# Kernel optimization log

Hardware: AMD Instinct MI355X
Metric: run time of the kernel (lower is better)

## Reference

```python
import jax, jax.numpy as jnp
import numpy as np

B, L, D = 2, 2048, 1024
H, QK, V = 8, 128, 128
EPS = 1e-5  # torch GroupNorm default


def setup_inputs() -> dict:
    key = jax.random.key(0)
    ks = jax.random.split(key, 6)
    sequence = jax.random.normal(ks[0], (B, L, D), jnp.float32)
    times = jnp.broadcast_to(jnp.arange(L, dtype=jnp.float32), (B, L))
    shift = D ** -0.5
    scale = 2.0 * shift
    w_q = jax.random.uniform(ks[1], (H, D, QK), jnp.float32) * scale - shift
    w_k = jax.random.uniform(ks[2], (H, D, QK), jnp.float32) * scale - shift
    w_v = jax.random.uniform(ks[3], (H, D, V), jnp.float32) * scale - shift
    out_dims = H * V
    w_g = jax.random.uniform(ks[4], (D, out_dims), jnp.float32) * scale - shift
    shift2 = out_dims ** -0.5
    scale2 = 2.0 * shift2
    w_o = jax.random.uniform(ks[5], (out_dims, out_dims), jnp.float32) * scale2 - shift2
    gn_w = jnp.ones((out_dims,), jnp.float32)
    gn_b = jnp.zeros((out_dims,), jnp.float32)
    return dict(sequence=sequence, times=times, w_q=w_q, w_k=w_k, w_v=w_v,
                w_g=w_g, w_o=w_o, gn_w=gn_w, gn_b=gn_b)


def rotate_by_i(x):
    # pairs (even, odd) -> (-odd, even), interleaved back
    x2 = x.reshape(x.shape[:-1] + (-1, 2))
    real, imag = x2[..., 0], x2[..., 1]
    return jnp.stack([-imag, real], axis=-1).reshape(x.shape)


def reference(sequence, times, w_q, w_k, w_v, w_g, w_o, gn_w, gn_b):
    gammas = 1.0 - 2.0 ** (-5.0 - jnp.arange(H, dtype=jnp.float32))            # (H,)
    thetas = 10000.0 ** (-2.0 * jnp.arange(QK // 2, dtype=jnp.float32) / QK)   # (QK/2,)

    q = jnp.einsum('bld,hdk->hblk', sequence, w_q)  # (H,B,L,QK)
    k = jnp.einsum('bld,hdk->hblk', sequence, w_k)
    v = jnp.einsum('bld,hdv->hblv', sequence, w_v)  # (H,B,L,V)

    # xPos rotor: angles interleaved-duplicated along last dim
    angles = times[..., None] * thetas              # (B,L,QK/2)
    cos = jnp.repeat(jnp.cos(angles), 2, axis=-1)   # (B,L,QK)
    sin = jnp.repeat(jnp.sin(angles), 2, axis=-1)
    q = cos * q + sin * rotate_by_i(q)
    k = cos * k - sin * rotate_by_i(k)

    # causal exponential-decay mask D[n,m] = gamma**(n-m) * (n>=m)
    mat = times[:, :, None] - times[:, None, :]     # (B,L,L)
    mask = mat >= 0
    g4 = gammas[:, None, None, None]                # (H,1,1,1)
    d = jnp.where(mask, g4 ** jnp.where(mask, mat, 0.0), 0.0)  # (H,B,L,L)

    ret = jnp.einsum('hbik,hbjk->hbij', q, k) * d   # (H,B,L,L)
    retention = jnp.einsum('hbij,hbjv->hbiv', ret, v)  # (H,B,L,V)

    # GroupNorm(num_heads, H*V): normalize each head's V channels per token
    r = jnp.transpose(retention, (1, 2, 0, 3))      # (B,L,H,V)
    mean = r.mean(-1, keepdims=True)
    var = r.var(-1, keepdims=True)
    rn = (r - mean) / jnp.sqrt(var + EPS)
    rn = rn * gn_w.reshape(H, V) + gn_b.reshape(H, V)
    rn = rn.reshape(B, L, H * V)

    g = sequence @ w_g
    gate = g * jax.nn.sigmoid(g)                    # swish
    return (gate * rn) @ w_o                        # (B,L,H*V)
```

## Files before the change

kernel.cpp:

```cpp
#include <hip/hip_runtime.h>
#include <stdint.h>

typedef unsigned short u16;
typedef unsigned int   u32;
typedef short  short8 __attribute__((ext_vector_type(8)));
typedef float  f32x4  __attribute__((ext_vector_type(4)));

#define DEV static __device__ __forceinline__

DEV float bf2f(u16 u) { u32 x = ((u32)u) << 16; float f; __builtin_memcpy(&f, &x, 4); return f; }
DEV u16 f2bf(float f) {
  u32 u; __builtin_memcpy(&u, &f, 4);
  return (u16)((u + 0x7FFFu + ((u >> 16) & 1u)) >> 16);
}
DEV bool probe_bf16(const void* times) { return *(const u32*)times == 0x3F800000u; }

DEV void gload16(const u16* g, u16* l) {
  __builtin_amdgcn_global_load_lds(
      (__attribute__((address_space(1))) void*)(u16*)g,
      (__attribute__((address_space(3))) void*)l, 16, 0, 0);
}

DEV f32x4 MFMA(short8 a, short8 b, f32x4 c) {
  return __builtin_amdgcn_mfma_f32_16x16x32_bf16(a, b, c, 0, 0, 0);
}

DEV void gemm128(const u16* Ag, const u16* Bg, int K, u16* sA, u16* sB,
                 f32x4 (&acc)[4][4]) {
  const int tid = threadIdx.x;
  const int lane = tid & 63, w = tid >> 6;
  const int wm = w >> 1, wn = w & 1;
  const int row = lane & 15, quad = lane >> 4;
  f32x4 z = {0.f, 0.f, 0.f, 0.f};
#pragma unroll
  for (int mt = 0; mt < 4; ++mt)
#pragma unroll
    for (int nt = 0; nt < 4; ++nt) acc[mt][nt] = z;

  for (int k0 = 0; k0 < K; k0 += 64) {
    __syncthreads();
#pragma unroll
    for (int i = 0; i < 4; ++i) {
      int c = (w << 2) + i;
      gload16(Ag + (size_t)(c * 8 + (lane >> 3)) * K + k0 + (lane & 7) * 8, sA + c * 544);
      gload16(Bg + (size_t)(c * 8 + (lane >> 3)) * K + k0 + (lane & 7) * 8, sB + c * 544);
    }
    __syncthreads();
#pragma unroll
    for (int kt = 0; kt < 2; ++kt) {
      short8 av[4], bv[4];
#pragma unroll
      for (int t = 0; t < 4; ++t) {
        int m = wm * 64 + t * 16 + row;
        av[t] = *(const short8*)(sA + (m >> 3) * 544 + (m & 7) * 64 + kt * 32 + quad * 8);
        int n = wn * 64 + t * 16 + row;
        bv[t] = *(const short8*)(sB + (n >> 3) * 544 + (n & 7) * 64 + kt * 32 + quad * 8);
      }
#pragma unroll
      for (int mt = 0; mt < 4; ++mt)
#pragma unroll
        for (int nt = 0; nt < 4; ++nt)
          acc[mt][nt] = MFMA(av[mt], bv[nt], acc[mt][nt]);
    }
  }
}

__global__ __launch_bounds__(256) void transpose_kernel(
    const void* wq, const void* wk, const void* wv, const void* wg,
    const void* wo, const void* times, u16* wsT) {
  __shared__ u16 T[128 * 132];
  int s = blockIdx.x, t = blockIdx.y;
  bool isbf = probe_bf16(times);
  const void* src; int ld; size_t off0;
  if (s < 8)       { src = wq; ld = 128;  off0 = (size_t)s * 131072; }
  else if (s < 16) { src = wk; ld = 128;  off0 = (size_t)(s - 8) * 131072; }
  else if (s < 24) { src = wv; ld = 128;  off0 = (size_t)(s - 16) * 131072; }
  else if (s < 32) { src = wg; ld = 1024; off0 = (size_t)(s - 24) * 128; }
  else             { src = wo; ld = 1024; off0 = (size_t)(s - 32) * 128; }
  int d0 = t * 128;
  const u16* s16 = (const u16*)src;
  const float* s32 = (const float*)src;
  for (int pass = 0; pass < 64; ++pass) {
    int idx = pass * 256 + threadIdx.x;
    int dl = idx >> 7, c = idx & 127;
    size_t goff = off0 + (size_t)(d0 + dl) * ld + c;
    T[c * 132 + dl] = isbf ? s16[goff] : f2bf(s32[goff]);
  }
  __syncthreads();
  u16* dst = wsT + (size_t)s * 131072;
  for (int pass = 0; pass < 16; ++pass) {
    int idx = pass * 256 + threadIdx.x;
    int c = idx >> 5, ch = idx & 31;
    uint2 v = *(const uint2*)&T[c * 132 + ch * 4];
    *(uint2*)&dst[(size_t)c * 1024 + d0 + ch * 4] = v;
  }
}

__global__ __launch_bounds__(256) void seq_kernel(const void* seq, const void* times, u16* dst) {
  bool isbf = probe_bf16(times);
  size_t idx = ((size_t)blockIdx.x * 256 + threadIdx.x) * 8;
  if (isbf) {
    *(uint4*)&dst[idx] = *(const uint4*)((const u16*)seq + idx);
  } else {
    const float* s = (const float*)seq;
    u32 a0 = (u32)f2bf(s[idx + 0]) | ((u32)f2bf(s[idx + 1]) << 16);
    u32 a1 = (u32)f2bf(s[idx + 2]) | ((u32)f2bf(s[idx + 3]) << 16);
    u32 a2 = (u32)f2bf(s[idx + 4]) | ((u32)f2bf(s[idx + 5]) << 16);
    u32 a3 = (u32)f2bf(s[idx + 6]) | ((u32)f2bf(s[idx + 7]) << 16);
    uint4 v; v.x = a0; v.y = a1; v.z = a2; v.w = a3;
    *(uint4*)&dst[idx] = v;
  }
}

__global__ __launch_bounds__(256, 4) void proj_kernel(
    const u16* seqb, const void* times, const u16* wsT,
    u16* qws, u16* kws, u16* vtws, u16* gatews) {
  __shared__ __align__(16) u16 smem[17408];
  u16* sA = smem;
  u16* sB = smem + 8704;
  int nb = blockIdx.x, mb = blockIdx.y;
  f32x4 acc[4][4];
  gemm128(seqb + (size_t)mb * 128 * 1024, wsT + (size_t)nb * 131072, 1024, sA, sB, acc);

  const int tid = threadIdx.x, lane = tid & 63, w = tid >> 6;
  const int wm = w >> 1, wn = w & 1, row = lane & 15, quad = lane >> 4;
  const bool isbf = probe_bf16(times);
  const u16* t16 = (const u16*)times;
  const float* t32 = (const float*)times;
  const int b = mb >> 4, l0 = (mb & 15) * 128;

  __syncthreads();

  if (nb < 16) {
    int type = nb >> 3;
    int h = nb & 7;
    float sgnk = type ? -1.f : 1.f;
#pragma unroll
    for (int mt = 0; mt < 4; ++mt) {
#pragma unroll
      for (int nt = 0; nt < 4; ++nt) {
        int c = wn * 64 + nt * 16 + row;
        float theta = exp2f(-0.2076205059304601f * (float)(c >> 1));
        float sgn = (c & 1) ? 1.f : -1.f;
#pragma unroll
        for (int r = 0; r < 4; ++r) {
          int lloc = wm * 64 + mt * 16 + quad * 4 + r;
          float v = acc[mt][nt][r];
          float pv = __shfl_xor(v, 1);
          float tv = isbf ? bf2f(t16[b * 2048 + l0 + lloc]) : t32[b * 2048 + l0 + lloc];
          float rev = theta * tv * 0.15915494309189535f;
          rev -= floorf(rev);
          float sn = __builtin_amdgcn_sinf(rev);
          float cs = __builtin_amdgcn_cosf(rev);
          float ov = cs * v + sgnk * sgn * sn * pv;
          u16 o16 = f2bf(ov);
          int other = __shfl_xor((int)o16, 1);
          if (!(lane & 1))
            *(u32*)&smem[lloc * 136 + c] = (u32)o16 | ((u32)other << 16);
        }
      }
    }
    __syncthreads();
    u16* outp = (type ? kws : qws) + (((size_t)(h * 2 + b) * 2048 + l0) << 7);
#pragma unroll
    for (int p = 0; p < 8; ++p) {
      int idx = p * 256 + tid, rr = idx >> 4, ch = idx & 15;
      *(uint4*)&outp[(size_t)rr * 128 + ch * 8] = *(const uint4*)&smem[rr * 136 + ch * 8];
    }
  } else if (nb < 24) {
    int h = nb & 7;
#pragma unroll
    for (int mt = 0; mt < 4; ++mt) {
      int lb = wm * 64 + mt * 16 + quad * 4;
#pragma unroll
      for (int nt = 0; nt < 4; ++nt) {
        int c = wn * 64 + nt * 16 + row;
        uint2 pk;
        pk.x = (u32)f2bf(acc[mt][nt][0]) | ((u32)f2bf(acc[mt][nt][1]) << 16);
        pk.y = (u32)f2bf(acc[mt][nt][2]) | ((u32)f2bf(acc[mt][nt][3]) << 16);
        *(uint2*)&smem[c * 136 + lb] = pk;
      }
    }
    __syncthreads();
    u16* outp = vtws + (size_t)(h * 2 + b) * 262144 + l0;
#pragma unroll
    for (int p = 0; p < 8; ++p) {
      int idx = p * 256 + tid, cc = idx >> 4, ch = idx & 15;
      *(uint4*)&outp[(size_t)cc * 2048 + ch * 8] = *(const uint4*)&smem[cc * 136 + ch * 8];
    }
  } else {
    int cb = nb - 24;
#pragma unroll
    for (int mt = 0; mt < 4; ++mt) {
#pragma unroll
      for (int nt = 0; nt < 4; ++nt) {
        int c = wn * 64 + nt * 16 + row;
#pragma unroll
        for (int r = 0; r < 4; ++r) {
          int lloc = wm * 64 + mt * 16 + quad * 4 + r;
          float x = acc[mt][nt][r];
          float s = x / (1.f + __expf(-x));
          u16 o16 = f2bf(s);
          int other = __shfl_xor((int)o16, 1);
          if (!(lane & 1))
            *(u32*)&smem[lloc * 136 + c] = (u32)o16 | ((u32)other << 16);
        }
      }
    }
    __syncthreads();
    u16* outp = gatews + (size_t)(mb * 128) * 1024 + (size_t)cb * 128;
#pragma unroll
    for (int p = 0; p < 8; ++p) {
      int idx = p * 256 + tid, rr = idx >> 4, ch = idx & 15;
      *(uint4*)&outp[(size_t)rr * 1024 + ch * 8] = *(const uint4*)&smem[rr * 136 + ch * 8];
    }
  }
}

__global__ __launch_bounds__(256) void retention_kernel(
    const u16* qws, const u16* kws, const u16* vtws, const void* times,
    float* rws, float* part0, float* part1) {
  __shared__ __align__(16) u16 sP[4][1280];
  const int tid = threadIdx.x, lane = tid & 63, w = tid >> 6;
  const int row = lane & 15, quad = lane >> 4;
  u16* myP = &sP[w][0];

  const int bx = blockIdx.x;
  const int xcd = bx & 7, slot = bx >> 3;
  const int hb = xcd + ((slot >> 5) << 3);
  const int cid = 125 - ((slot & 31) * 4 + w);
  if (cid < 0) return;
  int itile, idx, nc;
  if (cid < 22)      { itile = cid; idx = 0; nc = 1; }
  else if (cid < 66) { itile = 22 + ((cid - 22) >> 1); idx = (cid - 22) & 1; nc = 2; }
  else { int x = cid - 66; int q3 = (x * 171) >> 9; itile = 44 + q3; idx = x - 3 * q3; nc = 3; }
  const int n = itile + 1;
  int lo, hi;
  if (nc == 1)      { lo = 0;                      hi = n; }
  else if (nc == 2) { lo = (idx * n) >> 1;         hi = ((idx + 1) * n) >> 1; }
  else              { lo = (idx * n * 171) >> 9;   hi = ((idx + 1) * n * 171) >> 9; }

  const int h = hb >> 1, b = hb & 1;
  const int i0 = itile * 32;
  const bool isbf = probe_bf16(times);
  const u16* t16 = (const u16*)times + b * 2048;
  const float* t32 = (const float*)times + b * 2048;
  const float gamma = 1.f - exp2f(-5.f - (float)h);
  const float l2g = log2f(gamma);

  short8 qf[2][4];
  const u16* qbase = qws + ((size_t)hb * 2048 + i0) * 128;
#pragma unroll
  for (int ii = 0; ii < 2; ++ii)
#pragma unroll
    for (int kt = 0; kt < 4; ++kt)
      qf[ii][kt] = *(const short8*)(qbase + (size_t)(ii * 16 + row) * 128 + kt * 32 + quad * 8);

  float tiv[2];
#pragma unroll
  for (int ii = 0; ii < 2; ++ii)
    tiv[ii] = isbf ? bf2f(t16[i0 + ii * 16 + row]) : t32[i0 + ii * 16 + row];

  f32x4 z = {0.f, 0.f, 0.f, 0.f};
  f32x4 oacc[2][8];
#pragma unroll
  for (int mt = 0; mt < 2; ++mt)
#pragma unroll
    for (int vt = 0; vt < 8; ++vt) oacc[mt][vt] = z;

  const u16* kbase = kws + (size_t)hb * 262144;
  const u16* vbase = vtws + (size_t)hb * 262144;

  for (int jt = lo; jt < hi; ++jt) {
    const int j0 = jt * 32;
    if (l2g * (float)(i0 - j0 - 47) < -57.f) continue;

    f32x4 pt[2][2];
#pragma unroll
    for (int jj = 0; jj < 2; ++jj)
#pragma unroll
      for (int ii = 0; ii < 2; ++ii) pt[jj][ii] = z;
#pragma unroll
    for (int kt = 0; kt < 4; ++kt) {
      short8 kf0 = *(const short8*)(kbase + (size_t)(j0 + row) * 128 + kt * 32 + quad * 8);
      short8 kf1 = *(const short8*)(kbase + (size_t)(j0 + 16 + row) * 128 + kt * 32 + quad * 8);
      pt[0][0] = MFMA(kf0, qf[0][kt], pt[0][0]);
      pt[0][1] = MFMA(kf0, qf[1][kt], pt[0][1]);
      pt[1][0] = MFMA(kf1, qf[0][kt], pt[1][0]);
      pt[1][1] = MFMA(kf1, qf[1][kt], pt[1][1]);
    }

    const float j0f = (float)j0;
    const float rpo0 = exp2f(l2g * (tiv[0] - j0f));
    const float rpo1 = exp2f(l2g * (tiv[1] - j0f));
    const bool diag = (jt == itile);
#pragma unroll
    for (int jj = 0; jj < 2; ++jj) {
      float tj[4];
      if (isbf) {
        uint2 tp = *(const uint2*)&t16[j0 + jj * 16 + quad * 4];
        tj[0] = bf2f((u16)tp.x); tj[1] = bf2f((u16)(tp.x >> 16));
        tj[2] = bf2f((u16)tp.y); tj[3] = bf2f((u16)(tp.y >> 16));
      } else {
        f32x4 tp = *(const f32x4*)&t32[j0 + jj * 16 + quad * 4];
        tj[0] = tp[0]; tj[1] = tp[1]; tj[2] = tp[2]; tj[3] = tp[3];
      }
      float cp[4];
#pragma unroll
      for (int r = 0; r < 4; ++r) cp[r] = exp2f(l2g * (j0f - tj[r]));
#pragma unroll
      for (int ii = 0; ii < 2; ++ii) {
        float rp = ii ? rpo1 : rpo0;
        float ti = tiv[ii];
        float v0 = pt[jj][ii][0] * rp * cp[0];
        float v1 = pt[jj][ii][1] * rp * cp[1];
        float v2 = pt[jj][ii][2] * rp * cp[2];
        float v3 = pt[jj][ii][3] * rp * cp[3];
        if (diag) {
          if (ti < tj[0]) v0 = 0.f;
          if (ti < tj[1]) v1 = 0.f;
          if (ti < tj[2]) v2 = 0.f;
          if (ti < tj[3]) v3 = 0.f;
        }
        uint2 pk;
        pk.x = (u32)f2bf(v0) | ((u32)f2bf(v1) << 16);
        pk.y = (u32)f2bf(v2) | ((u32)f2bf(v3) << 16);
        *(uint2*)&myP[(ii * 16 + row) * 40 + jj * 16 + quad * 4] = pk;
      }
    }

    short8 a0 = *(const short8*)&myP[(row) * 40 + quad * 8];
    short8 a1 = *(const short8*)&myP[(16 + row) * 40 + quad * 8];
#pragma unroll
    for (int vt = 0; vt < 8; ++vt) {
      short8 vb = *(const short8*)(vbase + (size_t)(vt * 16 + row) * 2048 + j0 + quad * 8);
      oacc[0][vt] = MFMA(a0, vb, oacc[0][vt]);
      oacc[1][vt] = MFMA(a1, vb, oacc[1][vt]);
    }
  }

  float* dst;
  if (idx == 0) {
    dst = rws + ((size_t)hb * 2048 + i0) * 128;
  } else {
    int s_in = (itile < 44) ? (itile - 22) : (22 + (itile - 44) * 2 + (idx - 1));
    int s = hb * 62 + s_in;
    dst = (s < 512) ? part0 + (size_t)s * 4096 : part1 + (size_t)(s - 512) * 4096;
  }
#pragma unroll
  for (int mt = 0; mt < 2; ++mt)
#pragma unroll
    for (int vt = 0; vt < 8; ++vt)
#pragma unroll
      for (int r = 0; r < 4; ++r)
        dst[(size_t)(mt * 16 + quad * 4 + r) * 128 + vt * 16 + row] = oacc[mt][vt][r];
}

__global__ __launch_bounds__(256) void norm_kernel(
    const float* rws, const float* part0, const float* part1, const u16* gatews,
    const void* gnw, const void* gnb, const void* times, u16* xws) {
  int tid = threadIdx.x, lane = tid & 63, w = tid >> 6;
  int rid = blockIdx.x * 4 + w;
  int hb = rid >> 11, l = rid & 2047, h = hb >> 1, b = hb & 1;
  bool isbf = probe_bf16(times);
  float2 xv = *(const float2*)&rws[(size_t)rid * 128 + lane * 2];
  int it = l >> 5;
  if (it >= 22) {
    int s = hb * 62 + ((it < 44) ? (it - 22) : (22 + (it - 44) * 2));
    const float* pp = (s < 512) ? part0 + (size_t)s * 4096 : part1 + (size_t)(s - 512) * 4096;
    float2 x2 = *(const float2*)&pp[(l & 31) * 128 + lane * 2];
    xv.x += x2.x; xv.y += x2.y;
    if (it >= 44) {
      int s2 = s + 1;
      const float* pp2 = (s2 < 512) ? part0 + (size_t)s2 * 4096 : part1 + (size_t)(s2 - 512) * 4096;
      float2 x3 = *(const float2*)&pp2[(l & 31) * 128 + lane * 2];
      xv.x += x3.x; xv.y += x3.y;
    }
  }
  float s = xv.x + xv.y, ss = xv.x * xv.x + xv.y * xv.y;
#pragma unroll
  for (int o = 1; o < 64; o <<= 1) { s += __shfl_xor(s, o); ss += __shfl_xor(ss, o); }
  float mean = s * (1.f / 128.f);
  float var = fmaxf(ss * (1.f / 128.f) - mean * mean, 0.f);
  float inv = rsqrtf(var + 1e-5f);
  int c0 = h * 128 + lane * 2;
  float g0, g1, bb0, bb1;
  if (isbf) {
    g0 = bf2f(((const u16*)gnw)[c0]); g1 = bf2f(((const u16*)gnw)[c0 + 1]);
    bb0 = bf2f(((const u16*)gnb)[c0]); bb1 = bf2f(((const u16*)gnb)[c0 + 1]);
  } else {
    g0 = ((const float*)gnw)[c0]; g1 = ((const float*)gnw)[c0 + 1];
    bb0 = ((const float*)gnb)[c0]; bb1 = ((const float*)gnb)[c0 + 1];
  }
  float y0 = (xv.x - mean) * inv * g0 + bb0;
  float y1 = (xv.y - mean) * inv * g1 + bb1;
  size_t xi = ((size_t)(b * 2048 + l)) * 1024 + c0;
  float gt0 = bf2f(gatews[xi]), gt1 = bf2f(gatews[xi + 1]);
  u32 pk = (u32)f2bf(y0 * gt0) | ((u32)f2bf(y1 * gt1) << 16);
  *(u32*)&xws[xi] = pk;
}

__global__ __launch_bounds__(256, 4) void out_kernel(
    const u16* xws, const u16* wsT, const void* times, void* dout) {
  __shared__ __align__(16) u16 smem[17408];
  u16* sA = smem;
  u16* sB = smem + 8704;
  int nb = blockIdx.x, mb = blockIdx.y;
  f32x4 acc[4][4];
  gemm128(xws + (size_t)mb * 128 * 1024, wsT + (size_t)(32 + nb) * 131072, 1024, sA, sB, acc);
  const int tid = threadIdx.x, lane = tid & 63, w = tid >> 6;
  const int wm = w >> 1, wn = w & 1, row = lane & 15, quad = lane >> 4;
  bool isbf = probe_bf16(times);
  if (isbf) {
    __syncthreads();
#pragma unroll
    for (int mt = 0; mt < 4; ++mt) {
#pragma unroll
      for (int nt = 0; nt < 4; ++nt) {
        int c = wn * 64 + nt * 16 + row;
#pragma unroll
        for (int r = 0; r < 4; ++r) {
          int lloc = wm * 64 + mt * 16 + quad * 4 + r;
          u16 o16 = f2bf(acc[mt][nt][r]);
          int other = __shfl_xor((int)o16, 1);
          if (!(lane & 1))
            *(u32*)&smem[lloc * 136 + c] = (u32)o16 | ((u32)other << 16);
        }
      }
    }
    __syncthreads();
    u16* outp = (u16*)dout + (size_t)(mb * 128) * 1024 + (size_t)nb * 128;
#pragma unroll
    for (int p = 0; p < 8; ++p) {
      int idx = p * 256 + tid, rr = idx >> 4, ch = idx & 15;
      *(uint4*)&outp[(size_t)rr * 1024 + ch * 8] = *(const uint4*)&smem[rr * 136 + ch * 8];
    }
  } else {
#pragma unroll
    for (int mt = 0; mt < 4; ++mt)
#pragma unroll
      for (int nt = 0; nt < 4; ++nt)
#pragma unroll
        for (int r = 0; r < 4; ++r) {
          int i = mb * 128 + wm * 64 + mt * 16 + quad * 4 + r;
          size_t o = (size_t)i * 1024 + nb * 128 + wn * 64 + nt * 16 + row;
          ((float*)dout)[o] = acc[mt][nt][r];
        }
  }
}

extern "C" void kernel_launch(void* const* d_in, const int* in_sizes, int n_in,
                              void* d_out, int out_size, void* d_ws, size_t ws_size,
                              hipStream_t stream) {
  const void* seq   = d_in[0];
  const void* times = d_in[1];
  const void* wq = d_in[2];
  const void* wk = d_in[3];
  const void* wv = d_in[4];
  const void* wg = d_in[5];
  const void* wo = d_in[6];
  const void* gnw = d_in[7];
  const void* gnb = d_in[8];

  u16* ws = (u16*)d_ws;
  u16* wsT    = ws;
  u16* qws    = ws + 5242880;
  u16* kws    = qws + 4194304;
  u16* vtws   = kws + 4194304;
  u16* gatews = vtws + 4194304;
  float* rws  = (float*)(gatews + 4194304);
  u16* seqb   = (u16*)(rws + 4194304);
  float* part0 = (float*)seqb;
  float* part1 = (float*)wsT;
  u16* xws    = qws;

  transpose_kernel<<<dim3(40, 8), 256, 0, stream>>>(wq, wk, wv, wg, wo, times, wsT);
  seq_kernel<<<dim3(2048), 256, 0, stream>>>(seq, times, seqb);
  proj_kernel<<<dim3(32, 32), 256, 0, stream>>>(seqb, times, wsT, qws, kws, vtws, gatews);
  retention_kernel<<<dim3(512), 256, 0, stream>>>(qws, kws, vtws, times, rws, part0, part1);
  norm_kernel<<<dim3(8192), 256, 0, stream>>>(rws, part0, part1, gatews, gnw, gnb, times, xws);
  out_kernel<<<dim3(8, 32), 256, 0, stream>>>(xws, wsT, times, d_out);
}
```

Baseline: 291.4 us.

## Software-pipeline K tile loads and hoist V loads in retention loop

```diff
diff --git a/kernel.cpp b/kernel.cpp
--- a/kernel.cpp
+++ b/kernel.cpp
@@ -217,6 +217,99 @@
   }
 }
 
+DEV void ret_iter(
+    int jt, int hi, int itile,
+    const u16* kbase, const u16* vbase, const u16* t16, const float* t32,
+    bool isbf, int row, int quad, float l2g, float tiv0, float tiv1,
+    const short8 (&qf)[2][4], f32x4 (&oacc)[2][8], u16* myP,
+    short8 (&kcur)[8], short8 (&knxt)[8]) {
+  const int j0 = jt * 32;
+  const f32x4 z = {0.f, 0.f, 0.f, 0.f};
+
+  short8 vb[8];
+  {
+    const u16* vp = vbase + (size_t)row * 2048 + j0 + quad * 8;
+#pragma unroll
+    for (int vt = 0; vt < 8; ++vt)
+      vb[vt] = *(const short8*)(vp + (size_t)vt * 16 * 2048);
+  }
+  uint2 tp0 = {}, tp1 = {};
+  f32x4 tf0 = z, tf1 = z;
+  if (isbf) {
+    tp0 = *(const uint2*)&t16[j0 + quad * 4];
+    tp1 = *(const uint2*)&t16[j0 + 16 + quad * 4];
+  } else {
+    tf0 = *(const f32x4*)&t32[j0 + quad * 4];
+    tf1 = *(const f32x4*)&t32[j0 + 16 + quad * 4];
+  }
+
+  f32x4 pt[2][2] = {{z, z}, {z, z}};
+#pragma unroll
+  for (int kt = 0; kt < 4; ++kt) {
+    pt[0][0] = MFMA(kcur[kt], qf[0][kt], pt[0][0]);
+    pt[0][1] = MFMA(kcur[kt], qf[1][kt], pt[0][1]);
+    pt[1][0] = MFMA(kcur[4 + kt], qf[0][kt], pt[1][0]);
+    pt[1][1] = MFMA(kcur[4 + kt], qf[1][kt], pt[1][1]);
+  }
+
+  {
+    const int jn = (jt + 1 < hi) ? (jt + 1) : jt;
+    const u16* kp = kbase + (size_t)(jn * 32 + row) * 128 + quad * 8;
+#pragma unroll
+    for (int kt = 0; kt < 4; ++kt) {
+      knxt[kt] = *(const short8*)(kp + kt * 32);
+      knxt[4 + kt] = *(const short8*)(kp + 16 * 128 + kt * 32);
+    }
+  }
+
+  const float j0f = (float)j0;
+  const float rpo0 = exp2f(l2g * (tiv0 - j0f));
+  const float rpo1 = exp2f(l2g * (tiv1 - j0f));
+  const bool diag = (jt == itile);
+#pragma unroll
+  for (int jj = 0; jj < 2; ++jj) {
+    float tj[4];
+    if (isbf) {
+      uint2 tp = jj ? tp1 : tp0;
+      tj[0] = bf2f((u16)tp.x); tj[1] = bf2f((u16)(tp.x >> 16));
+      tj[2] = bf2f((u16)tp.y); tj[3] = bf2f((u16)(tp.y >> 16));
+    } else {
+      f32x4 tf = jj ? tf1 : tf0;
+      tj[0] = tf[0]; tj[1] = tf[1]; tj[2] = tf[2]; tj[3] = tf[3];
+    }
+    float cp[4];
+#pragma unroll
+    for (int r = 0; r < 4; ++r) cp[r] = exp2f(l2g * (j0f - tj[r]));
+#pragma unroll
+    for (int ii = 0; ii < 2; ++ii) {
+      float rp = ii ? rpo1 : rpo0;
+      float ti = ii ? tiv1 : tiv0;
+      float v0 = pt[jj][ii][0] * rp * cp[0];
+      float v1 = pt[jj][ii][1] * rp * cp[1];
+      float v2 = pt[jj][ii][2] * rp * cp[2];
+      float v3 = pt[jj][ii][3] * rp * cp[3];
+      if (diag) {
+        if (ti < tj[0]) v0 = 0.f;
+        if (ti < tj[1]) v1 = 0.f;
+        if (ti < tj[2]) v2 = 0.f;
+        if (ti < tj[3]) v3 = 0.f;
+      }
+      uint2 pk;
+      pk.x = (u32)f2bf(v0) | ((u32)f2bf(v1) << 16);
+      pk.y = (u32)f2bf(v2) | ((u32)f2bf(v3) << 16);
+      *(uint2*)&myP[(ii * 16 + row) * 40 + jj * 16 + quad * 4] = pk;
+    }
+  }
+
+  short8 a0 = *(const short8*)&myP[row * 40 + quad * 8];
+  short8 a1 = *(const short8*)&myP[(16 + row) * 40 + quad * 8];
+#pragma unroll
+  for (int vt = 0; vt < 8; ++vt) {
+    oacc[0][vt] = MFMA(a0, vb[vt], oacc[0][vt]);
+    oacc[1][vt] = MFMA(a1, vb[vt], oacc[1][vt]);
+  }
+}
+
 __global__ __launch_bounds__(256) void retention_kernel(
     const u16* qws, const u16* kws, const u16* vtws, const void* times,
     float* rws, float* part0, float* part1) {
@@ -248,6 +341,13 @@
   const float gamma = 1.f - exp2f(-5.f - (float)h);
   const float l2g = log2f(gamma);
 
+  int jt0 = lo;
+  {
+    float thr = (float)(i0 - 47) + 57.f / l2g;
+    int js = (int)ceilf(thr * (1.f / 32.f));
+    if (js > jt0) jt0 = js;
+  }
+
   short8 qf[2][4];
   const u16* qbase = qws + ((size_t)hb * 2048 + i0) * 128;
 #pragma unroll
@@ -256,10 +356,8 @@
     for (int kt = 0; kt < 4; ++kt)
       qf[ii][kt] = *(const short8*)(qbase + (size_t)(ii * 16 + row) * 128 + kt * 32 + quad * 8);
 
-  float tiv[2];
-#pragma unroll
-  for (int ii = 0; ii < 2; ++ii)
-    tiv[ii] = isbf ? bf2f(t16[i0 + ii * 16 + row]) : t32[i0 + ii * 16 + row];
+  float tiv0 = isbf ? bf2f(t16[i0 + row]) : t32[i0 + row];
+  float tiv1 = isbf ? bf2f(t16[i0 + 16 + row]) : t32[i0 + 16 + row];
 
   f32x4 z = {0.f, 0.f, 0.f, 0.f};
   f32x4 oacc[2][8];
@@ -271,73 +369,25 @@
   const u16* kbase = kws + (size_t)hb * 262144;
   const u16* vbase = vtws + (size_t)hb * 262144;
 
-  for (int jt = lo; jt < hi; ++jt) {
-    const int j0 = jt * 32;
-    if (l2g * (float)(i0 - j0 - 47) < -57.f) continue;
-
-    f32x4 pt[2][2];
-#pragma unroll
-    for (int jj = 0; jj < 2; ++jj)
-#pragma unroll
-      for (int ii = 0; ii < 2; ++ii) pt[jj][ii] = z;
+  short8 kc[8], kn[8];
+  int jt = jt0;
+  if (jt < hi) {
+    const u16* kp = kbase + (size_t)(jt * 32 + row) * 128 + quad * 8;
 #pragma unroll
     for (int kt = 0; kt < 4; ++kt) {
-      short8 kf0 = *(const short8*)(kbase + (size_t)(j0 + row) * 128 + kt * 32 + quad * 8);
-      short8 kf1 = *(const short8*)(kbase + (size_t)(j0 + 16 + row) * 128 + kt * 32 + quad * 8);
-      pt[0][0] = MFMA(kf0, qf[0][kt], pt[0][0]);
-      pt[0][1] = MFMA(kf0, qf[1][kt], pt[0][1]);
-      pt[1][0] = MFMA(kf1, qf[0][kt], pt[1][0]);
-      pt[1][1] = MFMA(kf1, qf[1][kt], pt[1][1]);
-    }
-
-    const float j0f = (float)j0;
-    const float rpo0 = exp2f(l2g * (tiv[0] - j0f));
-    const float rpo1 = exp2f(l2g * (tiv[1] - j0f));
-    const bool diag = (jt == itile);
-#pragma unroll
-    for (int jj = 0; jj < 2; ++jj) {
-      float tj[4];
-      if (isbf) {
-        uint2 tp = *(const uint2*)&t16[j0 + jj * 16 + quad * 4];
-        tj[0] = bf2f((u16)tp.x); tj[1] = bf2f((u16)(tp.x >> 16));
-        tj[2] = bf2f((u16)tp.y); tj[3] = bf2f((u16)(tp.y >> 16));
-      } else {
-        f32x4 tp = *(const f32x4*)&t32[j0 + jj * 16 + quad * 4];
-        tj[0] = tp[0]; tj[1] = tp[1]; tj[2] = tp[2]; tj[3] = tp[3];
-      }
-      float cp[4];
-#pragma unroll
-      for (int r = 0; r < 4; ++r) cp[r] = exp2f(l2g * (j0f - tj[r]));
-#pragma unroll
-      for (int ii = 0; ii < 2; ++ii) {
-        float rp = ii ? rpo1 : rpo0;
-        float ti = tiv[ii];
-        float v0 = pt[jj][ii][0] * rp * cp[0];
-        float v1 = pt[jj][ii][1] * rp * cp[1];
-        float v2 = pt[jj][ii][2] * rp * cp[2];
-        float v3 = pt[jj][ii][3] * rp * cp[3];
-        if (diag) {
-          if (ti < tj[0]) v0 = 0.f;
-          if (ti < tj[1]) v1 = 0.f;
-          if (ti < tj[2]) v2 = 0.f;
-          if (ti < tj[3]) v3 = 0.f;
-        }
-        uint2 pk;
-        pk.x = (u32)f2bf(v0) | ((u32)f2bf(v1) << 16);
-        pk.y = (u32)f2bf(v2) | ((u32)f2bf(v3) << 16);
-        *(uint2*)&myP[(ii * 16 + row) * 40 + jj * 16 + quad * 4] = pk;
-      }
-    }
-
-    short8 a0 = *(const short8*)&myP[(row) * 40 + quad * 8];
-    short8 a1 = *(const short8*)&myP[(16 + row) * 40 + quad * 8];
-#pragma unroll
-    for (int vt = 0; vt < 8; ++vt) {
-      short8 vb = *(const short8*)(vbase + (size_t)(vt * 16 + row) * 2048 + j0 + quad * 8);
-      oacc[0][vt] = MFMA(a0, vb, oacc[0][vt]);
-      oacc[1][vt] = MFMA(a1, vb, oacc[1][vt]);
-    }
-  }
+      kc[kt] = *(const short8*)(kp + kt * 32);
+      kc[4 + kt] = *(const short8*)(kp + 16 * 128 + kt * 32);
+    }
+  }
+  for (; jt + 1 < hi; jt += 2) {
+    ret_iter(jt, hi, itile, kbase, vbase, t16, t32, isbf, row, quad,
+             l2g, tiv0, tiv1, qf, oacc, myP, kc, kn);
+    ret_iter(jt + 1, hi, itile, kbase, vbase, t16, t32, isbf, row, quad,
+             l2g, tiv0, tiv1, qf, oacc, myP, kn, kc);
+  }
+  if (jt < hi)
+    ret_iter(jt, hi, itile, kbase, vbase, t16, t32, isbf, row, quad,
+             l2g, tiv0, tiv1, qf, oacc, myP, kc, kn);
 
   float* dst;
   if (idx == 0) {
```

New measurement: 283.8 us. -2.6%, faster.
